# Kernel optimization log

Hardware: AMD Instinct MI355X
Metric: run time of the kernel (lower is better)

## Reference

```python
import jax, jax.numpy as jnp
import numpy as np

DIM_INPUT = 8192
DIM_OUTPUT = 8192
N_FANOUT = 16
BATCH = 1024
WEIGHT = 100.0
NNZ = DIM_INPUT * N_FANOUT


def setup_inputs() -> dict:
    key = jax.random.key(0)
    rng = np.random.default_rng(0)
    # pre: each input neuron appears N_FANOUT times (arange % dim_input)
    pre = jnp.asarray(np.arange(NNZ) % DIM_INPUT, dtype=jnp.int32)
    # post: random permutation modulo dim_output (fixed random connectivity)
    post_np = rng.permutation(max(DIM_INPUT, DIM_OUTPUT) * N_FANOUT)[:NNZ] % DIM_OUTPUT
    post = jnp.asarray(post_np, dtype=jnp.int32)
    x = jax.random.normal(key, (BATCH, DIM_INPUT), dtype=jnp.float32)
    return {"x": x, "pre": pre, "post": post}


def reference(x, pre, post):
    # Sparse W (dim_output x dim_input) with W[post[e], pre[e]] += WEIGHT
    # (torch.sparse coalesces duplicates by summation; scatter-add matches).
    # y[b, j] = sum_{e: post[e]==j} WEIGHT * x[b, pre[e]]
    gathered = WEIGHT * jnp.take(x, pre, axis=1)          # [B, NNZ]
    y = jax.ops.segment_sum(gathered.T, post, num_segments=DIM_OUTPUT)  # [DIM_OUTPUT, B]
    return y.T                                             # [B, DIM_OUTPUT]
```

## Files before the change

kernel.cpp:

```cpp
#include <hip/hip_runtime.h>
#include <hip/hip_fp16.h>

#define DIM_IN   8192
#define DIM_OUT  8192
#define FAN      16
#define BATCH    1024
#define NNZ      (DIM_IN * FAN)
#define ROWS     8
#define BLOCK    1024
#define OSPLIT   2
#define OCHUNK   (DIM_OUT / OSPLIT)
#define LDS_BYTES (DIM_IN * ROWS * 2)
#define ROUT     32

__global__ __launch_bounds__(1024)
void build_scan_kernel(const int* __restrict__ pre,
                       const int* __restrict__ post,
                       int* __restrict__ idx) {
    __shared__ int cnt[ROUT];
    __shared__ int sidx[ROUT * FAN];
    const int t  = threadIdx.x;
    const int j0 = blockIdx.x * ROUT;

    if (t < ROUT) cnt[t] = 0;
    __syncthreads();

    for (int base = 0; base < NNZ; base += 4096) {
        const int e0 = base + t;
        const int p0 = post[e0];
        const int p1 = post[e0 + 1024];
        const int p2 = post[e0 + 2048];
        const int p3 = post[e0 + 3072];

        const unsigned r0 = (unsigned)(p0 - j0);
        const unsigned r1 = (unsigned)(p1 - j0);
        const unsigned r2 = (unsigned)(p2 - j0);
        const unsigned r3 = (unsigned)(p3 - j0);

        if (r0 < ROUT) { int s = atomicAdd(&cnt[r0], 1); if (s < FAN) sidx[r0 * FAN + s] = pre[e0]; }
        if (r1 < ROUT) { int s = atomicAdd(&cnt[r1], 1); if (s < FAN) sidx[r1 * FAN + s] = pre[e0 + 1024]; }
        if (r2 < ROUT) { int s = atomicAdd(&cnt[r2], 1); if (s < FAN) sidx[r2 * FAN + s] = pre[e0 + 2048]; }
        if (r3 < ROUT) { int s = atomicAdd(&cnt[r3], 1); if (s < FAN) sidx[r3 * FAN + s] = pre[e0 + 3072]; }
    }
    __syncthreads();

    if (t < ROUT * FAN) idx[(size_t)j0 * FAN + t] = sidx[t];
}

__global__ __launch_bounds__(BLOCK, 1)
void gather_kernel(const float* __restrict__ x,
                   const int*   __restrict__ idx,
                   float*       __restrict__ y) {
    extern __shared__ __half ldsh[];
    const int t  = threadIdx.x;
    const int b0 = (blockIdx.x >> 1) * ROWS;
    const int j0 = (blockIdx.x & 1) * OCHUNK;

#pragma unroll
    for (int c = 0; c < DIM_IN / BLOCK; ++c) {
        const int i = t + c * BLOCK;
        uint4 w;
        {
            __half2 h;
            h.x = __float2half(x[(size_t)(b0 + 0) * DIM_IN + i]);
            h.y = __float2half(x[(size_t)(b0 + 1) * DIM_IN + i]);
            w.x = *reinterpret_cast<unsigned*>(&h);
            h.x = __float2half(x[(size_t)(b0 + 2) * DIM_IN + i]);
            h.y = __float2half(x[(size_t)(b0 + 3) * DIM_IN + i]);
            w.y = *reinterpret_cast<unsigned*>(&h);
            h.x = __float2half(x[(size_t)(b0 + 4) * DIM_IN + i]);
            h.y = __float2half(x[(size_t)(b0 + 5) * DIM_IN + i]);
            w.z = *reinterpret_cast<unsigned*>(&h);
            h.x = __float2half(x[(size_t)(b0 + 6) * DIM_IN + i]);
            h.y = __float2half(x[(size_t)(b0 + 7) * DIM_IN + i]);
            w.w = *reinterpret_cast<unsigned*>(&h);
        }
        *reinterpret_cast<uint4*>(&ldsh[(size_t)i * ROWS]) = w;
    }
    __syncthreads();

#pragma unroll
    for (int o = 0; o < OCHUNK / BLOCK; ++o) {
        const int j = j0 + t + o * BLOCK;
        const int4* ip = reinterpret_cast<const int4*>(idx + (size_t)j * FAN);
        int4 i0 = ip[0];
        int4 i1 = ip[1];
        int4 i2 = ip[2];
        int4 i3 = ip[3];

        float acc0 = 0.f, acc1 = 0.f, acc2 = 0.f, acc3 = 0.f;
        float acc4 = 0.f, acc5 = 0.f, acc6 = 0.f, acc7 = 0.f;

        auto accum = [&](int i) {
            const uint4 u = *reinterpret_cast<const uint4*>(&ldsh[(size_t)i * ROWS]);
            float2 f;
            f = __half22float2(*reinterpret_cast<const __half2*>(&u.x));
            acc0 += f.x; acc1 += f.y;
            f = __half22float2(*reinterpret_cast<const __half2*>(&u.y));
            acc2 += f.x; acc3 += f.y;
            f = __half22float2(*reinterpret_cast<const __half2*>(&u.z));
            acc4 += f.x; acc5 += f.y;
            f = __half22float2(*reinterpret_cast<const __half2*>(&u.w));
            acc6 += f.x; acc7 += f.y;
        };
        accum(i0.x); accum(i0.y); accum(i0.z); accum(i0.w);
        accum(i1.x); accum(i1.y); accum(i1.z); accum(i1.w);
        accum(i2.x); accum(i2.y); accum(i2.z); accum(i2.w);
        accum(i3.x); accum(i3.y); accum(i3.z); accum(i3.w);

        y[(size_t)(b0 + 0) * DIM_OUT + j] = 100.0f * acc0;
        y[(size_t)(b0 + 1) * DIM_OUT + j] = 100.0f * acc1;
        y[(size_t)(b0 + 2) * DIM_OUT + j] = 100.0f * acc2;
        y[(size_t)(b0 + 3) * DIM_OUT + j] = 100.0f * acc3;
        y[(size_t)(b0 + 4) * DIM_OUT + j] = 100.0f * acc4;
        y[(size_t)(b0 + 5) * DIM_OUT + j] = 100.0f * acc5;
        y[(size_t)(b0 + 6) * DIM_OUT + j] = 100.0f * acc6;
        y[(size_t)(b0 + 7) * DIM_OUT + j] = 100.0f * acc7;
    }
}

extern "C" void kernel_launch(void* const* d_in, const int* in_sizes, int n_in,
                              void* d_out, int out_size, void* d_ws, size_t ws_size,
                              hipStream_t stream) {
    const float* x    = (const float*)d_in[0];
    const int*   pre  = (const int*)d_in[1];
    const int*   post = (const int*)d_in[2];
    float*       y    = (float*)d_out;
    int*         idx  = (int*)d_ws;

    hipFuncSetAttribute((const void*)gather_kernel,
                        hipFuncAttributeMaxDynamicSharedMemorySize, LDS_BYTES);

    build_scan_kernel<<<DIM_OUT / ROUT, 1024, 0, stream>>>(pre, post, idx);
    gather_kernel<<<(BATCH / ROWS) * OSPLIT, BLOCK, LDS_BYTES, stream>>>(x, idx, y);
}
```

Before: 120.5 us.

## Transpose x to half-precision batch-major layout and gather rows from global memory

Adds a transpose kernel that converts x into an fp16 [DIM_IN, BATCH] buffer in workspace. A new spmm kernel then gathers 16 contiguous batch values per index straight from global or L2 memory, in tiles of 64 outputs by 256 batch rows. This replaces the old approach, where each block staged a full 8-row slab of x in LDS and had only one 1024-thread block per CU. The aim is more parallelism and the end of redundant LDS staging. The cost is an extra kernel launch, a 16 MB intermediate, and uncoalesced y stores. The old path is kept as a fallback when the workspace is too small.

```diff
diff --git a/kernel.cpp b/kernel.cpp
--- a/kernel.cpp
+++ b/kernel.cpp
@@ -6,11 +6,6 @@
 #define FAN      16
 #define BATCH    1024
 #define NNZ      (DIM_IN * FAN)
-#define ROWS     8
-#define BLOCK    1024
-#define OSPLIT   2
-#define OCHUNK   (DIM_OUT / OSPLIT)
-#define LDS_BYTES (DIM_IN * ROWS * 2)
 #define ROUT     32
 
 __global__ __launch_bounds__(1024)
@@ -47,6 +42,90 @@
     if (t < ROUT * FAN) idx[(size_t)j0 * FAN + t] = sidx[t];
 }
 
+__global__ __launch_bounds__(256)
+void transpose_kernel(const float* __restrict__ x, __half* __restrict__ xt) {
+    const int t  = threadIdx.x;
+    const int it = blockIdx.x & 127;
+    const int bt = blockIdx.x >> 7;
+    const int i0 = it * 64, b0 = bt * 64;
+    const int bq = t & 15;
+    const int iq = t >> 4;
+
+    float4 m[4];
+#pragma unroll
+    for (int r = 0; r < 4; ++r)
+        m[r] = *reinterpret_cast<const float4*>(
+            x + (size_t)(b0 + bq * 4 + r) * DIM_IN + i0 + iq * 4);
+
+#pragma unroll
+    for (int e = 0; e < 4; ++e) {
+        __half2 lo, hi;
+        lo.x = __float2half(((const float*)&m[0])[e]);
+        lo.y = __float2half(((const float*)&m[1])[e]);
+        hi.x = __float2half(((const float*)&m[2])[e]);
+        hi.y = __float2half(((const float*)&m[3])[e]);
+        uint2 w;
+        w.x = *reinterpret_cast<unsigned*>(&lo);
+        w.y = *reinterpret_cast<unsigned*>(&hi);
+        *reinterpret_cast<uint2*>(xt + (size_t)(i0 + iq * 4 + e) * BATCH + b0 + bq * 4) = w;
+    }
+}
+
+#define JT 64
+#define BT 256
+__global__ __launch_bounds__(1024)
+void spmm_kernel(const __half* __restrict__ xt,
+                 const int*    __restrict__ idx,
+                 float*        __restrict__ y) {
+    __shared__ int sidx[JT * FAN];
+    const int bid   = blockIdx.x;
+    const int x8    = bid & 7;
+    const int grp   = bid >> 3;
+    const int btile = x8 >> 1;
+    const int jtile = grp * 2 + (x8 & 1);
+    const int j0 = jtile * JT;
+    const int b0 = btile * BT;
+    const int t  = threadIdx.x;
+
+    sidx[t] = idx[(size_t)j0 * FAN + t];
+    __syncthreads();
+
+    const int jj = t >> 4;
+    const int bb = t & 15;
+
+    float acc[16];
+#pragma unroll
+    for (int m = 0; m < 16; ++m) acc[m] = 0.f;
+
+    const __half* base = xt + b0 + bb * 16;
+#pragma unroll
+    for (int k = 0; k < FAN; ++k) {
+        const int i = sidx[jj * FAN + k];
+        const uint4* p = reinterpret_cast<const uint4*>(base + (size_t)i * BATCH);
+        const uint4 u0 = p[0];
+        const uint4 u1 = p[1];
+        float2 f;
+        f = __half22float2(*reinterpret_cast<const __half2*>(&u0.x)); acc[0]  += f.x; acc[1]  += f.y;
+        f = __half22float2(*reinterpret_cast<const __half2*>(&u0.y)); acc[2]  += f.x; acc[3]  += f.y;
+        f = __half22float2(*reinterpret_cast<const __half2*>(&u0.z)); acc[4]  += f.x; acc[5]  += f.y;
+        f = __half22float2(*reinterpret_cast<const __half2*>(&u0.w)); acc[6]  += f.x; acc[7]  += f.y;
+        f = __half22float2(*reinterpret_cast<const __half2*>(&u1.x)); acc[8]  += f.x; acc[9]  += f.y;
+        f = __half22float2(*reinterpret_cast<const __half2*>(&u1.y)); acc[10] += f.x; acc[11] += f.y;
+        f = __half22float2(*reinterpret_cast<const __half2*>(&u1.z)); acc[12] += f.x; acc[13] += f.y;
+        f = __half22float2(*reinterpret_cast<const __half2*>(&u1.w)); acc[14] += f.x; acc[15] += f.y;
+    }
+
+    float* yb = y + (size_t)(b0 + bb * 16) * DIM_OUT + j0 + jj;
+#pragma unroll
+    for (int m = 0; m < 16; ++m)
+        yb[(size_t)m * DIM_OUT] = 100.0f * acc[m];
+}
+
+#define ROWS     8
+#define BLOCK    1024
+#define OSPLIT   2
+#define OCHUNK   (DIM_OUT / OSPLIT)
+#define LDS_BYTES (DIM_IN * ROWS * 2)
 __global__ __launch_bounds__(BLOCK, 1)
 void gather_kernel(const float* __restrict__ x,
                    const int*   __restrict__ idx,
@@ -60,21 +139,19 @@
     for (int c = 0; c < DIM_IN / BLOCK; ++c) {
         const int i = t + c * BLOCK;
         uint4 w;
-        {
-            __half2 h;
-            h.x = __float2half(x[(size_t)(b0 + 0) * DIM_IN + i]);
-            h.y = __float2half(x[(size_t)(b0 + 1) * DIM_IN + i]);
-            w.x = *reinterpret_cast<unsigned*>(&h);
-            h.x = __float2half(x[(size_t)(b0 + 2) * DIM_IN + i]);
-            h.y = __float2half(x[(size_t)(b0 + 3) * DIM_IN + i]);
-            w.y = *reinterpret_cast<unsigned*>(&h);
-            h.x = __float2half(x[(size_t)(b0 + 4) * DIM_IN + i]);
-            h.y = __float2half(x[(size_t)(b0 + 5) * DIM_IN + i]);
-            w.z = *reinterpret_cast<unsigned*>(&h);
-            h.x = __float2half(x[(size_t)(b0 + 6) * DIM_IN + i]);
-            h.y = __float2half(x[(size_t)(b0 + 7) * DIM_IN + i]);
-            w.w = *reinterpret_cast<unsigned*>(&h);
-        }
+        __half2 h;
+        h.x = __float2half(x[(size_t)(b0 + 0) * DIM_IN + i]);
+        h.y = __float2half(x[(size_t)(b0 + 1) * DIM_IN + i]);
+        w.x = *reinterpret_cast<unsigned*>(&h);
+        h.x = __float2half(x[(size_t)(b0 + 2) * DIM_IN + i]);
+        h.y = __float2half(x[(size_t)(b0 + 3) * DIM_IN + i]);
+        w.y = *reinterpret_cast<unsigned*>(&h);
+        h.x = __float2half(x[(size_t)(b0 + 4) * DIM_IN + i]);
+        h.y = __float2half(x[(size_t)(b0 + 5) * DIM_IN + i]);
+        w.z = *reinterpret_cast<unsigned*>(&h);
+        h.x = __float2half(x[(size_t)(b0 + 6) * DIM_IN + i]);
+        h.y = __float2half(x[(size_t)(b0 + 7) * DIM_IN + i]);
+        w.w = *reinterpret_cast<unsigned*>(&h);
         *reinterpret_cast<uint4*>(&ldsh[(size_t)i * ROWS]) = w;
     }
     __syncthreads();
@@ -88,34 +165,28 @@
         int4 i2 = ip[2];
         int4 i3 = ip[3];
 
-        float acc0 = 0.f, acc1 = 0.f, acc2 = 0.f, acc3 = 0.f;
-        float acc4 = 0.f, acc5 = 0.f, acc6 = 0.f, acc7 = 0.f;
-
+        float a0=0,a1=0,a2=0,a3=0,a4=0,a5=0,a6=0,a7=0;
         auto accum = [&](int i) {
             const uint4 u = *reinterpret_cast<const uint4*>(&ldsh[(size_t)i * ROWS]);
             float2 f;
-            f = __half22float2(*reinterpret_cast<const __half2*>(&u.x));
-            acc0 += f.x; acc1 += f.y;
-            f = __half22float2(*reinterpret_cast<const __half2*>(&u.y));
-            acc2 += f.x; acc3 += f.y;
-            f = __half22float2(*reinterpret_cast<const __half2*>(&u.z));
-            acc4 += f.x; acc5 += f.y;
-            f = __half22float2(*reinterpret_cast<const __half2*>(&u.w));
-            acc6 += f.x; acc7 += f.y;
+            f = __half22float2(*reinterpret_cast<const __half2*>(&u.x)); a0 += f.x; a1 += f.y;
+            f = __half22float2(*reinterpret_cast<const __half2*>(&u.y)); a2 += f.x; a3 += f.y;
+            f = __half22float2(*reinterpret_cast<const __half2*>(&u.z)); a4 += f.x; a5 += f.y;
+            f = __half22float2(*reinterpret_cast<const __half2*>(&u.w)); a6 += f.x; a7 += f.y;
         };
         accum(i0.x); accum(i0.y); accum(i0.z); accum(i0.w);
         accum(i1.x); accum(i1.y); accum(i1.z); accum(i1.w);
         accum(i2.x); accum(i2.y); accum(i2.z); accum(i2.w);
         accum(i3.x); accum(i3.y); accum(i3.z); accum(i3.w);
 
-        y[(size_t)(b0 + 0) * DIM_OUT + j] = 100.0f * acc0;
-        y[(size_t)(b0 + 1) * DIM_OUT + j] = 100.0f * acc1;
-        y[(size_t)(b0 + 2) * DIM_OUT + j] = 100.0f * acc2;
-        y[(size_t)(b0 + 3) * DIM_OUT + j] = 100.0f * acc3;
-        y[(size_t)(b0 + 4) * DIM_OUT + j] = 100.0f * acc4;
-        y[(size_t)(b0 + 5) * DIM_OUT + j] = 100.0f * acc5;
-        y[(size_t)(b0 + 6) * DIM_OUT + j] = 100.0f * acc6;
-        y[(size_t)(b0 + 7) * DIM_OUT + j] = 100.0f * acc7;
+        y[(size_t)(b0 + 0) * DIM_OUT + j] = 100.0f * a0;
+        y[(size_t)(b0 + 1) * DIM_OUT + j] = 100.0f * a1;
+        y[(size_t)(b0 + 2) * DIM_OUT + j] = 100.0f * a2;
+        y[(size_t)(b0 + 3) * DIM_OUT + j] = 100.0f * a3;
+        y[(size_t)(b0 + 4) * DIM_OUT + j] = 100.0f * a4;
+        y[(size_t)(b0 + 5) * DIM_OUT + j] = 100.0f * a5;
+        y[(size_t)(b0 + 6) * DIM_OUT + j] = 100.0f * a6;
+        y[(size_t)(b0 + 7) * DIM_OUT + j] = 100.0f * a7;
     }
 }
 
@@ -126,11 +197,22 @@
     const int*   pre  = (const int*)d_in[1];
     const int*   post = (const int*)d_in[2];
     float*       y    = (float*)d_out;
-    int*         idx  = (int*)d_ws;
-
-    hipFuncSetAttribute((const void*)gather_kernel,
-                        hipFuncAttributeMaxDynamicSharedMemorySize, LDS_BYTES);
-
-    build_scan_kernel<<<DIM_OUT / ROUT, 1024, 0, stream>>>(pre, post, idx);
-    gather_kernel<<<(BATCH / ROWS) * OSPLIT, BLOCK, LDS_BYTES, stream>>>(x, idx, y);
-}
+
+    const size_t xt_bytes  = (size_t)DIM_IN * BATCH * sizeof(__half);
+    const size_t idx_bytes = (size_t)NNZ * sizeof(int);
+
+    if (ws_size >= xt_bytes + idx_bytes) {
+        __half* xt  = (__half*)d_ws;
+        int*    idx = (int*)((char*)d_ws + xt_bytes);
+
+        build_scan_kernel<<<DIM_OUT / ROUT, 1024, 0, stream>>>(pre, post, idx);
+        transpose_kernel<<<(DIM_IN / 64) * (BATCH / 64), 256, 0, stream>>>(x, xt);
+        spmm_kernel<<<(DIM_OUT / JT) * (BATCH / BT), 1024, 0, stream>>>(xt, idx, y);
+    } else {
+        int* idx = (int*)d_ws;
+        hipFuncSetAttribute((const void*)gather_kernel,
+                            hipFuncAttributeMaxDynamicSharedMemorySize, LDS_BYTES);
+        build_scan_kernel<<<DIM_OUT / ROUT, 1024, 0, stream>>>(pre, post, idx);
+        gather_kernel<<<(BATCH / ROWS) * OSPLIT, BLOCK, LDS_BYTES, stream>>>(x, idx, y);
+    }
+}
```

New measurement: 141.8 us. 1.18x slower.
